# Performance work log

Measured on AMD Instinct MI355X. Metric: run time of the kernel, lower is better.

The kernel has to match this reference:

```python
import jax, jax.numpy as jnp
import numpy as np

B, N, C, H = 8, 2048, 768, 12
HD = C // H
SCALE = HD ** -0.5


def setup_inputs() -> dict:
    key = jax.random.key(0)
    ks = jax.random.split(key, 10)
    x = jax.random.normal(ks[0], (B, N, C), dtype=jnp.float32)
    size = jax.random.uniform(ks[1], (B, N, 1), dtype=jnp.float32, minval=0.1, maxval=8.0)
    def lin(k):
        return jax.random.normal(k, (C, C), dtype=jnp.float32) * 0.02
    return {
        "x": x,
        "size": size,
        "q_w": lin(ks[2]), "q_b": jnp.zeros((C,), jnp.float32),
        "k_w": lin(ks[3]), "k_b": jnp.zeros((C,), jnp.float32),
        "v_w": lin(ks[4]), "v_b": jnp.zeros((C,), jnp.float32),
        "o_w": lin(ks[5]), "o_b": jnp.zeros((C,), jnp.float32),
    }


def reference(x, size, q_w, q_b, k_w, k_b, v_w, v_b, o_w, o_b):
    # q/k/v projections: [B,N,C] -> [B,H,N,hd]
    def proj(w, b):
        y = jnp.einsum('bnc,dc->bnd', x, w) + b
        return y.reshape(B, N, H, HD).transpose(0, 2, 1, 3)
    q = proj(q_w, q_b)
    k = proj(k_w, k_b)
    v = proj(v_w, v_b)
    # scores with additive log-size bias on keys: [B,H,N,N]
    attn = jnp.einsum('bhqd,bhkd->bhqk', q, k) * SCALE
    attn = attn + jnp.log(size)[:, None, None, :, 0]
    attn = jax.nn.softmax(attn, axis=-1)
    out = jnp.einsum('bhqk,bhkd->bhqd', attn, v)
    out = out.transpose(0, 2, 1, 3).reshape(B, N, C)
    out = jnp.einsum('bnc,dc->bnd', out, o_w) + o_b
    return out, k.mean(axis=1)
```

## Files before the change

kernel.cpp:

```cpp
#include <hip/hip_runtime.h>
#include <math.h>

constexpr int BB = 8, NN = 2048, CC = 768, HH = 12, DD = 64;
constexpr float SCALE2 = 0.18033688011112042f;
constexpr long long BNC = (long long)BB * NN * CC;
constexpr long long WN  = 589824LL;
constexpr long long XN  = BNC;

using bf16x8  = __attribute__((ext_vector_type(8))) __bf16;
using floatx4 = __attribute__((ext_vector_type(4))) float;
using f16x4   = __attribute__((ext_vector_type(4))) _Float16;
using f16x8   = __attribute__((ext_vector_type(8))) _Float16;

static __device__ __forceinline__ unsigned short f2bf(float x) {
  unsigned u = __builtin_bit_cast(unsigned, x);
  u += 0x7fffu + ((u >> 16) & 1u);
  return (unsigned short)(u >> 16);
}
static __device__ __forceinline__ float bf2f(unsigned short s) {
  unsigned u = ((unsigned)s) << 16;
  return __builtin_bit_cast(float, u);
}

static __device__ __forceinline__ void async_copy16(const unsigned short* g, unsigned short* l) {
  __builtin_amdgcn_global_load_lds(
      (const __attribute__((address_space(1))) unsigned int*)g,
      (__attribute__((address_space(3))) unsigned int*)l, 16, 0, 0);
}

__global__ void convert_kernel(const float* __restrict__ x,
    const float* __restrict__ qw, const float* __restrict__ kw,
    const float* __restrict__ vw, const float* __restrict__ ow,
    const float* __restrict__ qb, const float* __restrict__ kb,
    const float* __restrict__ vb,
    unsigned short* __restrict__ xb, unsigned short* __restrict__ wcat,
    unsigned short* __restrict__ owb, float* __restrict__ bcat) {
  const long long gid = (long long)blockIdx.x * 256 + threadIdx.x;
  const long long off = gid * 4;
  if (off < XN + 4 * WN) {
    const float* s; unsigned short* d;
    if (off < XN)              { s = x  + off;                 d = xb   + off; }
    else if (off < XN + WN)    { s = qw + (off - XN);          d = wcat + (off - XN); }
    else if (off < XN + 2*WN)  { s = kw + (off - XN - WN);     d = wcat + (off - XN); }
    else if (off < XN + 3*WN)  { s = vw + (off - XN - 2*WN);   d = wcat + (off - XN); }
    else                       { s = ow + (off - XN - 3*WN);   d = owb  + (off - XN - 3*WN); }
    floatx4 v = *(const floatx4*)s;
    union { unsigned short us[4]; unsigned long long u; } pk;
    pk.us[0] = f2bf(v.x); pk.us[1] = f2bf(v.y); pk.us[2] = f2bf(v.z); pk.us[3] = f2bf(v.w);
    *(unsigned long long*)d = pk.u;
  } else {
    long long r = gid - (XN + 4 * WN) / 4;
    if (r < 576) {
      long long o2 = r * 4;
      const float* s = (o2 < 768) ? qb + o2 : (o2 < 1536) ? kb + (o2 - 768) : vb + (o2 - 1536);
      *(floatx4*)(bcat + o2) = *(const floatx4*)s;
    }
  }
}

template<int OUT_MODE>
__global__ __launch_bounds__(256, 3)
void gemm_m97(const unsigned short* __restrict__ A,
              const unsigned short* __restrict__ Bw,
              const float* __restrict__ bias,
              unsigned short* __restrict__ Qo,
              unsigned short* __restrict__ Ko,
              unsigned short* __restrict__ Vo,
              float* __restrict__ Fo) {
  __shared__ __align__(16) unsigned short As[128 * 64];
  __shared__ __align__(16) unsigned short Bs[128 * 64];
  const int t    = threadIdx.x;
  const int lane = t & 63;
  const int wv   = t >> 6;
  const int q    = lane >> 4;
  const int ml   = lane & 15;
  const int wm   = wv >> 1, wn = wv & 1;
  const int m0   = blockIdx.x * 128;
  const int n0   = blockIdx.y * 128;
  const int scol = ((lane & 7) ^ (lane >> 3)) * 8;

  const unsigned short* Ag = A  + (size_t)(m0 + wv * 32 + (lane >> 3)) * CC + scol;
  const unsigned short* Bg = Bw + (size_t)(n0 + wv * 32 + (lane >> 3)) * CC + scol;
  unsigned short* Al = As + (wv * 32) * 64;
  unsigned short* Bl = Bs + (wv * 32) * 64;

  floatx4 acc[4][4] = {};

  for (int k0 = 0; k0 < CC; k0 += 64) {
    #pragma unroll
    for (int i = 0; i < 4; ++i) {
      async_copy16(Ag + (size_t)i * 8 * CC + k0, Al + i * 8 * 64);
      async_copy16(Bg + (size_t)i * 8 * CC + k0, Bl + i * 8 * 64);
    }
    __syncthreads();
    #pragma unroll
    for (int kk = 0; kk < 2; ++kk) {
      bf16x8 af[4], bg[4];
      #pragma unroll
      for (int mt = 0; mt < 4; ++mt) {
        const int ch = ((kk * 4 + q) ^ (ml & 7)) * 8;
        af[mt] = *(const bf16x8*)&As[(wm * 64 + mt * 16 + ml) * 64 + ch];
      }
      #pragma unroll
      for (int nt = 0; nt < 4; ++nt) {
        const int ch = ((kk * 4 + q) ^ (ml & 7)) * 8;
        bg[nt] = *(const bf16x8*)&Bs[(wn * 64 + nt * 16 + ml) * 64 + ch];
      }
      #pragma unroll
      for (int mt = 0; mt < 4; ++mt)
        #pragma unroll
        for (int nt = 0; nt < 4; ++nt)
          acc[mt][nt] = __builtin_amdgcn_mfma_f32_16x16x32_bf16(af[mt], bg[nt], acc[mt][nt], 0, 0, 0);
    }
    __syncthreads();
  }

  #pragma unroll
  for (int nt = 0; nt < 4; ++nt) {
    const int col = n0 + wn * 64 + nt * 16 + ml;
    const float bv = bias[col];
    #pragma unroll
    for (int mt = 0; mt < 4; ++mt) {
      const int mbase = m0 + wm * 64 + mt * 16 + q * 4;
      if (OUT_MODE == 1) {
        #pragma unroll
        for (int r = 0; r < 4; ++r)
          Fo[(size_t)(mbase + r) * CC + col] = acc[mt][nt][r] + bv;
      } else {
        const int region = blockIdx.y / 6;
        const int lc = col - region * CC;
        const int h = lc >> 6, hd = lc & 63;
        const int bidx = mbase >> 11;
        if (region == 2) {
          const int nloc  = mbase & (NN - 1);
          const int pbase = (nloc & ~127) + (((nloc >> 2) & 3) << 5) + (((nloc >> 4) & 7) << 2);
          union { _Float16 h4[4]; unsigned long long u; } pk;
          #pragma unroll
          for (int r = 0; r < 4; ++r) pk.h4[r] = (_Float16)(acc[mt][nt][r] + bv);
          *(unsigned long long*)&Vo[((size_t)(bidx * HH + h) * DD + hd) * NN + pbase] = pk.u;
        } else {
          const int n = mbase & (NN - 1);
          unsigned short* o = (region == 0) ? Qo : Ko;
          #pragma unroll
          for (int r = 0; r < 4; ++r)
            o[((size_t)(bidx * HH + h) * NN + n + r) * DD + hd] = f2bf(acc[mt][nt][r] + bv);
        }
      }
    }
  }
}

__global__ __launch_bounds__(256, 2)
void attn_kernel(const unsigned short* __restrict__ Qp,
                 const unsigned short* __restrict__ Kp,
                 const unsigned short* __restrict__ Vt,
                 const float* __restrict__ sz,
                 unsigned short* __restrict__ attn_out) {
  __shared__ __align__(16) unsigned short Ks[2][128 * 64];
  __shared__ __align__(16) unsigned short Vs[64 * 128];
  __shared__ __align__(16) float biasS[2][128];

  const int t    = threadIdx.x;
  const int lane = t & 63;
  const int wv   = t >> 6;
  const int q    = lane >> 4;
  const int ml   = lane & 15;
  const int wg   = (blockIdx.x & 7) * 192 + (blockIdx.x >> 3);
  const int bh   = wg >> 4;
  const int qt   = wg & 15;
  const int b    = bh / HH, h = bh % HH;
  const int qbase = qt * 128 + wv * 32;

  bf16x8 qf[2][2];
  #pragma unroll
  for (int mq = 0; mq < 2; ++mq)
    #pragma unroll
    for (int kt = 0; kt < 2; ++kt)
      qf[mq][kt] = *(const bf16x8*)(Qp + ((size_t)bh * NN + qbase + mq * 16 + ml) * DD + kt * 32 + q * 8);

  floatx4 O[2][4] = {};
  floatx4 Osum[2] = {};
  f16x8 vone8 = {(_Float16)1.f, (_Float16)1.f, (_Float16)1.f, (_Float16)1.f,
                 (_Float16)1.f, (_Float16)1.f, (_Float16)1.f, (_Float16)1.f};

  const int kswz = ((lane & 7) ^ (lane >> 3)) * 8;
  const int vswz = ((lane & 15) ^ (lane >> 4)) * 8;
  const unsigned short* Kg = Kp + ((size_t)bh * NN + wv * 32 + (lane >> 3)) * DD + kswz;
  const unsigned short* Vg = Vt + ((size_t)bh * DD + wv * 16 + (lane >> 4)) * NN;
  unsigned short* Kl0 = &Ks[0][(wv * 32) * 64];
  unsigned short* Kl1 = &Ks[1][(wv * 32) * 64];
  unsigned short* Vl  = Vs + (wv * 16) * 128;

  #pragma unroll
  for (int i = 0; i < 4; ++i) {
    async_copy16(Kg + (size_t)(i * 8) * DD, Kl0 + i * 8 * 64);
    async_copy16(Vg + (size_t)(i * 4) * NN + (vswz ^ ((i & 1) << 5)), Vl + i * 4 * 128);
  }
  float szreg = 0.f;
  if (t < 128) {
    biasS[0][t] = log2f(sz[(size_t)b * NN + t]);
    szreg = sz[(size_t)b * NN + 128 + t];
  }
  __syncthreads();

  for (int jt = 0; jt < 16; ++jt) {
    const int cur = jt & 1;
    const int j0  = jt * 128;
    const int jn  = j0 + 128;
    unsigned short* Kln = cur ? Kl0 : Kl1;

    if (jt < 15) {
      #pragma unroll
      for (int i = 0; i < 4; ++i)
        async_copy16(Kg + (size_t)(jn + i * 8) * DD, Kln + i * 8 * 64);
      if (t < 128) {
        biasS[cur ^ 1][t] = log2f(szreg);
        int j2 = jn + 128; if (j2 + 128 > NN) j2 = NN - 128;
        szreg = sz[(size_t)b * NN + j2 + t];
      }
    }

    floatx4 bfr[8];
    #pragma unroll
    for (int nt = 0; nt < 8; ++nt)
      bfr[nt] = *(const floatx4*)&biasS[cur][nt * 16 + q * 4];

    floatx4 S[2][8];
    __builtin_amdgcn_s_setprio(1);
    #pragma unroll
    for (int nt = 0; nt < 8; ++nt) {
      const int ch0 = (q ^ (ml & 7)) * 8;
      const int ch1 = ((4 + q) ^ (ml & 7)) * 8;
      bf16x8 kf0 = *(const bf16x8*)&Ks[cur][(nt * 16 + ml) * 64 + ch0];
      bf16x8 kf1 = *(const bf16x8*)&Ks[cur][(nt * 16 + ml) * 64 + ch1];
      #pragma unroll
      for (int mq = 0; mq < 2; ++mq) {
        floatx4 a = {0.f, 0.f, 0.f, 0.f};
        a = __builtin_amdgcn_mfma_f32_16x16x32_bf16(kf0, qf[mq][0], a, 0, 0, 0);
        a = __builtin_amdgcn_mfma_f32_16x16x32_bf16(kf1, qf[mq][1], a, 0, 0, 0);
        S[mq][nt] = a;
      }
    }
    __builtin_amdgcn_s_setprio(0);

    f16x8 pfw[2][4];
    #pragma unroll
    for (int mq = 0; mq < 2; ++mq)
      #pragma unroll
      for (int tt = 0; tt < 4; ++tt)
        #pragma unroll
        for (int bb = 0; bb < 2; ++bb)
          #pragma unroll
          for (int r = 0; r < 4; ++r)
            pfw[mq][tt][bb * 4 + r] =
                (_Float16)__builtin_amdgcn_exp2f(fmaf(S[mq][2 * tt + bb][r], SCALE2, bfr[2 * tt + bb][r]));

    __syncthreads();

    __builtin_amdgcn_s_setprio(1);
    #pragma unroll
    for (int dt = 0; dt < 4; ++dt) {
      #pragma unroll
      for (int tt = 0; tt < 4; ++tt) {
        const int ch = ((q * 4 + tt) ^ (ml & 7)) * 8;
        f16x8 vv = *(const f16x8*)&Vs[(dt * 16 + ml) * 128 + ch];
        #pragma unroll
        for (int mq = 0; mq < 2; ++mq)
          O[mq][dt] = __builtin_amdgcn_mfma_f32_16x16x32_f16(vv, pfw[mq][tt], O[mq][dt], 0, 0, 0);
      }
    }
    __builtin_amdgcn_s_setprio(0);

    __syncthreads();

    if (jt < 15) {
      #pragma unroll
      for (int i = 0; i < 4; ++i)
        async_copy16(Vg + (size_t)(i * 4) * NN + jn + (vswz ^ ((i & 1) << 5)), Vl + i * 4 * 128);
    }

    __builtin_amdgcn_s_setprio(1);
    #pragma unroll
    for (int mq = 0; mq < 2; ++mq)
      #pragma unroll
      for (int tt = 0; tt < 4; ++tt)
        Osum[mq] = __builtin_amdgcn_mfma_f32_16x16x32_f16(vone8, pfw[mq][tt], Osum[mq], 0, 0, 0);
    __builtin_amdgcn_s_setprio(0);
  }

  #pragma unroll
  for (int mq = 0; mq < 2; ++mq) {
    const float linv = 1.0f / Osum[mq][0];
    const int query = qbase + mq * 16 + ml;
    #pragma unroll
    for (int dt = 0; dt < 4; ++dt) {
      union { unsigned short us[4]; unsigned long long u; } pk;
      #pragma unroll
      for (int r = 0; r < 4; ++r) pk.us[r] = f2bf(O[mq][dt][r] * linv);
      *(unsigned long long*)&attn_out[((size_t)b * NN + query) * CC + h * DD + dt * 16 + q * 4] = pk.u;
    }
  }
}

__global__ void kmean_kernel(const unsigned short* __restrict__ Kp, float* __restrict__ o) {
  int idx = blockIdx.x * 256 + threadIdx.x;
  int hd4 = (idx & 15) << 2;
  int n   = (idx >> 4) & (NN - 1);
  int b   = idx >> 15;
  float s0 = 0.f, s1 = 0.f, s2 = 0.f, s3 = 0.f;
  #pragma unroll
  for (int h = 0; h < HH; ++h) {
    ushort4 u = *(const ushort4*)&Kp[(((size_t)b * HH + h) * NN + n) * DD + hd4];
    s0 += bf2f(u.x); s1 += bf2f(u.y); s2 += bf2f(u.z); s3 += bf2f(u.w);
  }
  float4 r;
  r.x = s0 * (1.0f / 12.0f); r.y = s1 * (1.0f / 12.0f);
  r.z = s2 * (1.0f / 12.0f); r.w = s3 * (1.0f / 12.0f);
  *(float4*)&o[(size_t)idx * 4] = r;
}

extern "C" void kernel_launch(void* const* d_in, const int* in_sizes, int n_in,
                              void* d_out, int out_size, void* d_ws, size_t ws_size,
                              hipStream_t stream) {
  const float* x   = (const float*)d_in[0];
  const float* sz  = (const float*)d_in[1];
  const float* q_w = (const float*)d_in[2];
  const float* q_b = (const float*)d_in[3];
  const float* k_w = (const float*)d_in[4];
  const float* k_b = (const float*)d_in[5];
  const float* v_w = (const float*)d_in[6];
  const float* v_b = (const float*)d_in[7];
  const float* o_w = (const float*)d_in[8];
  const float* o_b = (const float*)d_in[9];

  float* out0  = (float*)d_out;
  float* outKm = out0 + (size_t)BNC;

  unsigned short* xb   = (unsigned short*)d_ws;
  unsigned short* wcat = xb + XN;
  unsigned short* owb  = wcat + 3 * WN;
  float*          bcat = (float*)(owb + WN);
  unsigned short* Qw   = (unsigned short*)(bcat + 2304);
  unsigned short* Kw   = Qw + BNC;
  unsigned short* Vtw  = Kw + BNC;
  unsigned short* Aw   = xb;

  dim3 tb(256, 1, 1);
  convert_kernel<<<dim3(14595), tb, 0, stream>>>(x, q_w, k_w, v_w, o_w, q_b, k_b, v_b,
                                                 xb, wcat, owb, bcat);
  gemm_m97<0><<<dim3(128, 18), tb, 0, stream>>>(xb, wcat, bcat, Qw, Kw, Vtw, nullptr);
  attn_kernel<<<dim3(BB * HH * 16), tb, 0, stream>>>(Qw, Kw, Vtw, sz, Aw);
  gemm_m97<1><<<dim3(128, 6), tb, 0, stream>>>(Aw, owb, o_b, nullptr, nullptr, nullptr, out0);
  kmean_kernel<<<dim3(1024), tb, 0, stream>>>(Kw, outKm);
}
```

Baseline: 341.4 us.

## Halve attention query tile to 64 rows and raise occupancy to 3 blocks/SM

Each attention workgroup now handles 64 queries (16 per wave) instead of 128, doubling the grid to 3072 blocks. Score computation is split into two phases of four key subtiles to shrink live registers, and launch bounds are raised to allow three resident blocks per CU. The aim is more latency hiding and better load balance. The cost is that K and V tiles are loaded from global memory twice as often per query, and each loaded K/V fragment is reused across half as many MFMAs.

```diff
diff --git a/kernel.cpp b/kernel.cpp
--- a/kernel.cpp
+++ b/kernel.cpp
@@ -150,7 +150,7 @@
   }
 }
 
-__global__ __launch_bounds__(256, 2)
+__global__ __launch_bounds__(256, 3)
 void attn_kernel(const unsigned short* __restrict__ Qp,
                  const unsigned short* __restrict__ Kp,
                  const unsigned short* __restrict__ Vt,
@@ -165,21 +165,19 @@
   const int wv   = t >> 6;
   const int q    = lane >> 4;
   const int ml   = lane & 15;
-  const int wg   = (blockIdx.x & 7) * 192 + (blockIdx.x >> 3);
-  const int bh   = wg >> 4;
-  const int qt   = wg & 15;
+  const int wg   = (blockIdx.x & 7) * 384 + (blockIdx.x >> 3);
+  const int bh   = wg >> 5;
+  const int qt   = wg & 31;
   const int b    = bh / HH, h = bh % HH;
-  const int qbase = qt * 128 + wv * 32;
-
-  bf16x8 qf[2][2];
+  const int qbase = qt * 64 + wv * 16;
+
+  bf16x8 qf[2];
   #pragma unroll
-  for (int mq = 0; mq < 2; ++mq)
-    #pragma unroll
-    for (int kt = 0; kt < 2; ++kt)
-      qf[mq][kt] = *(const bf16x8*)(Qp + ((size_t)bh * NN + qbase + mq * 16 + ml) * DD + kt * 32 + q * 8);
-
-  floatx4 O[2][4] = {};
-  floatx4 Osum[2] = {};
+  for (int kt = 0; kt < 2; ++kt)
+    qf[kt] = *(const bf16x8*)(Qp + ((size_t)bh * NN + qbase + ml) * DD + kt * 32 + q * 8);
+
+  floatx4 O[4] = {};
+  floatx4 Osum = {};
   f16x8 vone8 = {(_Float16)1.f, (_Float16)1.f, (_Float16)1.f, (_Float16)1.f,
                  (_Float16)1.f, (_Float16)1.f, (_Float16)1.f, (_Float16)1.f};
 
@@ -205,8 +203,7 @@
 
   for (int jt = 0; jt < 16; ++jt) {
     const int cur = jt & 1;
-    const int j0  = jt * 128;
-    const int jn  = j0 + 128;
+    const int jn  = jt * 128 + 128;
     unsigned short* Kln = cur ? Kl0 : Kl1;
 
     if (jt < 15) {
@@ -220,40 +217,38 @@
       }
     }
 
-    floatx4 bfr[8];
-    #pragma unroll
-    for (int nt = 0; nt < 8; ++nt)
-      bfr[nt] = *(const floatx4*)&biasS[cur][nt * 16 + q * 4];
-
-    floatx4 S[2][8];
-    __builtin_amdgcn_s_setprio(1);
-    #pragma unroll
-    for (int nt = 0; nt < 8; ++nt) {
-      const int ch0 = (q ^ (ml & 7)) * 8;
-      const int ch1 = ((4 + q) ^ (ml & 7)) * 8;
-      bf16x8 kf0 = *(const bf16x8*)&Ks[cur][(nt * 16 + ml) * 64 + ch0];
-      bf16x8 kf1 = *(const bf16x8*)&Ks[cur][(nt * 16 + ml) * 64 + ch1];
-      #pragma unroll
-      for (int mq = 0; mq < 2; ++mq) {
+    f16x8 pfw[4];
+    #pragma unroll
+    for (int ph = 0; ph < 2; ++ph) {
+      floatx4 S[4];
+      __builtin_amdgcn_s_setprio(1);
+      #pragma unroll
+      for (int nt2 = 0; nt2 < 4; ++nt2) {
+        const int nt  = ph * 4 + nt2;
+        const int ch0 = (q ^ (ml & 7)) * 8;
+        const int ch1 = ((4 + q) ^ (ml & 7)) * 8;
+        bf16x8 kf0 = *(const bf16x8*)&Ks[cur][(nt * 16 + ml) * 64 + ch0];
+        bf16x8 kf1 = *(const bf16x8*)&Ks[cur][(nt * 16 + ml) * 64 + ch1];
         floatx4 a = {0.f, 0.f, 0.f, 0.f};
-        a = __builtin_amdgcn_mfma_f32_16x16x32_bf16(kf0, qf[mq][0], a, 0, 0, 0);
-        a = __builtin_amdgcn_mfma_f32_16x16x32_bf16(kf1, qf[mq][1], a, 0, 0, 0);
-        S[mq][nt] = a;
-      }
-    }
-    __builtin_amdgcn_s_setprio(0);
-
-    f16x8 pfw[2][4];
-    #pragma unroll
-    for (int mq = 0; mq < 2; ++mq)
-      #pragma unroll
-      for (int tt = 0; tt < 4; ++tt)
+        a = __builtin_amdgcn_mfma_f32_16x16x32_bf16(kf0, qf[0], a, 0, 0, 0);
+        a = __builtin_amdgcn_mfma_f32_16x16x32_bf16(kf1, qf[1], a, 0, 0, 0);
+        S[nt2] = a;
+      }
+      __builtin_amdgcn_s_setprio(0);
+      #pragma unroll
+      for (int tt2 = 0; tt2 < 2; ++tt2) {
+        const int tt = ph * 2 + tt2;
         #pragma unroll
-        for (int bb = 0; bb < 2; ++bb)
+        for (int bb = 0; bb < 2; ++bb) {
+          const int nt = ph * 4 + tt2 * 2 + bb;
+          floatx4 bv = *(const floatx4*)&biasS[cur][nt * 16 + q * 4];
           #pragma unroll
           for (int r = 0; r < 4; ++r)
-            pfw[mq][tt][bb * 4 + r] =
-                (_Float16)__builtin_amdgcn_exp2f(fmaf(S[mq][2 * tt + bb][r], SCALE2, bfr[2 * tt + bb][r]));
+            pfw[tt][bb * 4 + r] =
+                (_Float16)__builtin_amdgcn_exp2f(fmaf(S[tt2 * 2 + bb][r], SCALE2, bv[r]));
+        }
+      }
+    }
 
     __syncthreads();
 
@@ -264,9 +259,7 @@
       for (int tt = 0; tt < 4; ++tt) {
         const int ch = ((q * 4 + tt) ^ (ml & 7)) * 8;
         f16x8 vv = *(const f16x8*)&Vs[(dt * 16 + ml) * 128 + ch];
-        #pragma unroll
-        for (int mq = 0; mq < 2; ++mq)
-          O[mq][dt] = __builtin_amdgcn_mfma_f32_16x16x32_f16(vv, pfw[mq][tt], O[mq][dt], 0, 0, 0);
+        O[dt] = __builtin_amdgcn_mfma_f32_16x16x32_f16(vv, pfw[tt], O[dt], 0, 0, 0);
       }
     }
     __builtin_amdgcn_s_setprio(0);
@@ -281,22 +274,19 @@
 
     __builtin_amdgcn_s_setprio(1);
     #pragma unroll
-    for (int mq = 0; mq < 2; ++mq)
-      #pragma unroll
-      for (int tt = 0; tt < 4; ++tt)
-        Osum[mq] = __builtin_amdgcn_mfma_f32_16x16x32_f16(vone8, pfw[mq][tt], Osum[mq], 0, 0, 0);
+    for (int tt = 0; tt < 4; ++tt)
+      Osum = __builtin_amdgcn_mfma_f32_16x16x32_f16(vone8, pfw[tt], Osum, 0, 0, 0);
     __builtin_amdgcn_s_setprio(0);
   }
 
-  #pragma unroll
-  for (int mq = 0; mq < 2; ++mq) {
-    const float linv = 1.0f / Osum[mq][0];
-    const int query = qbase + mq * 16 + ml;
+  {
+    const float linv = 1.0f / Osum[0];
+    const int query = qbase + ml;
     #pragma unroll
     for (int dt = 0; dt < 4; ++dt) {
       union { unsigned short us[4]; unsigned long long u; } pk;
       #pragma unroll
-      for (int r = 0; r < 4; ++r) pk.us[r] = f2bf(O[mq][dt][r] * linv);
+      for (int r = 0; r < 4; ++r) pk.us[r] = f2bf(O[dt][r] * linv);
       *(unsigned long long*)&attn_out[((size_t)b * NN + query) * CC + h * DD + dt * 16 + q * 4] = pk.u;
     }
   }
@@ -349,7 +339,7 @@
   convert_kernel<<<dim3(14595), tb, 0, stream>>>(x, q_w, k_w, v_w, o_w, q_b, k_b, v_b,
                                                  xb, wcat, owb, bcat);
   gemm_m97<0><<<dim3(128, 18), tb, 0, stream>>>(xb, wcat, bcat, Qw, Kw, Vtw, nullptr);
-  attn_kernel<<<dim3(BB * HH * 16), tb, 0, stream>>>(Qw, Kw, Vtw, sz, Aw);
+  attn_kernel<<<dim3(3072), tb, 0, stream>>>(Qw, Kw, Vtw, sz, Aw);
   gemm_m97<1><<<dim3(128, 6), tb, 0, stream>>>(Aw, owb, o_b, nullptr, nullptr, nullptr, out0);
   kmean_kernel<<<dim3(1024), tb, 0, stream>>>(Kw, outKm);
 }
```

Measured after the change: 353.2 us. 1.03x slower.
